# Optimization experiments

Measured on AMD Instinct MI355X. Metric: run time of the kernel, lower is better.

## Reference

```python
import jax, jax.numpy as jnp
import numpy as np

NUM_HEADS = 8
BN_EPS = 1e-3  # keras BatchNormalization default epsilon


def setup_inputs() -> dict:
    key = jax.random.key(0)
    ks = jax.random.split(key, 4)
    B, N, C, s, H = 8, 1024, 3, 16, NUM_HEADS
    dim = s * s * C  # 768
    return {
        "x": jax.random.normal(ks[0], (B, N, dim), jnp.float32),
        "qconv_w": jax.random.normal(ks[1], (3, 3, C, C), jnp.float32) * 0.1,  # HWIO, shared q/k/v (source bug, faithful)
        "reatten_w": jax.random.normal(ks[2], (H, H), jnp.float32) * 0.2,      # 1x1 conv mixing heads
        "reatten_b": jnp.zeros((H,), jnp.float32),
        "bn_gamma": jnp.ones((H,), jnp.float32),
        "bn_beta": jnp.zeros((H,), jnp.float32),
        "bn_mean": jnp.zeros((H,), jnp.float32),
        "bn_var": jnp.ones((H,), jnp.float32),
        "proj_w": jax.random.normal(ks[3], (dim, dim), jnp.float32) * 0.02,
        "proj_b": jnp.zeros((dim,), jnp.float32),
    }


def reference(x, qconv_w, reatten_w, reatten_b, bn_gamma, bn_beta, bn_mean, bn_var, proj_w, proj_b):
    H = NUM_HEADS
    B, N, P = x.shape
    C = qconv_w.shape[2]
    s = int(np.sqrt(P // C))
    hd = P // H
    scale = hd ** -0.5

    # unflatten: tokens become conv batch; 3x3 same conv, no bias
    xim = x.reshape(B * N, s, s, C)
    y = jax.lax.conv_general_dilated(
        xim, qconv_w, window_strides=(1, 1), padding='SAME',
        dimension_numbers=('NHWC', 'HWIO', 'NHWC'))
    # source applies qconv2d for q, k AND v -> identical projections
    q = y.reshape(B, N, H, hd).transpose(0, 2, 1, 3)  # [B,H,N,hd]

    attn = jax.nn.softmax(jnp.einsum('bhnd,bhmd->bhnm', q, q) * scale, axis=-1)

    # re-attention: 1x1 conv across heads + inference batchnorm (per head channel), reatten_scale=1.0
    re = jnp.einsum('bhnm,hg->bgnm', attn, reatten_w) + reatten_b[None, :, None, None]
    st = lambda a: a[None, :, None, None]
    attn_next = (re - st(bn_mean)) * st(bn_gamma) / jnp.sqrt(st(bn_var) + BN_EPS) + st(bn_beta)

    out = jnp.einsum('bgnm,bgmd->bngd', attn_next, q).reshape(B, N, P)
    xo = out @ proj_w + proj_b
    return (xo, attn_next)
```

## Files before the change

kernel.cpp:

```cpp
#include <hip/hip_runtime.h>

#define NB 8
#define NN 1024
#define NH 8
#define HD 96
#define DIM 768

typedef __bf16 bf16x8 __attribute__((ext_vector_type(8)));
typedef float f32x4 __attribute__((ext_vector_type(4)));
typedef unsigned short u16x8 __attribute__((ext_vector_type(8)));

__device__ __forceinline__ ushort f2bf(float f) {
  uint u = __float_as_uint(f);
  u += 0x7fffu + ((u >> 16) & 1u);
  return (ushort)(u >> 16);
}
__device__ __forceinline__ float bf2f(ushort u) {
  return __uint_as_float(((uint)u) << 16);
}

__global__ __launch_bounds__(256) void k_prep_w(const float* __restrict__ pw,
                                                ushort* __restrict__ wT) {
  __shared__ ushort tile[64][72];
  int d0 = blockIdx.x * 64;
  int j0 = blockIdx.y * 64;
  int t = threadIdx.x;
  {
    int r = t >> 2;
    int ch = (t & 3) * 16;
    const float* src = pw + (size_t)(d0 + r) * DIM + j0 + ch;
#pragma unroll
    for (int i = 0; i < 16; i += 4) {
      float4 v = *(const float4*)(src + i);
      tile[ch + i + 0][r] = f2bf(v.x);
      tile[ch + i + 1][r] = f2bf(v.y);
      tile[ch + i + 2][r] = f2bf(v.z);
      tile[ch + i + 3][r] = f2bf(v.w);
    }
  }
  __syncthreads();
  {
    int j = t >> 2;
    int ch = (t & 3) * 16;
    union { ushort u[16]; uint4 v[2]; } tmp;
#pragma unroll
    for (int i = 0; i < 16; ++i) tmp.u[i] = tile[j][ch + i];
    uint4* dst = (uint4*)(wT + (size_t)(j0 + j) * DIM + d0 + ch);
    dst[0] = tmp.v[0]; dst[1] = tmp.v[1];
  }
}

__global__ __launch_bounds__(256) void k_conv(const float* __restrict__ x,
                                              const float* __restrict__ w,
                                              ushort* __restrict__ q) {
  __shared__ float xs[768];
  __shared__ float ws[81];
  __shared__ ushort os[768];
  int token = blockIdx.x;
  int t = threadIdx.x;
  const float4* xin = (const float4*)(x + (size_t)token * DIM);
  if (t < 192) ((float4*)xs)[t] = xin[t];
  if (t < 81) ws[t] = w[t];
  __syncthreads();
  int r = t >> 4, c = t & 15;
  float a0 = 0.f, a1 = 0.f, a2 = 0.f;
#pragma unroll
  for (int dr = 0; dr < 3; ++dr) {
    int rr = r + dr - 1;
    bool rok = (rr >= 0) & (rr < 16);
#pragma unroll
    for (int dc = 0; dc < 3; ++dc) {
      int cc = c + dc - 1;
      bool ok = rok & (cc >= 0) & (cc < 16);
#pragma unroll
      for (int ci = 0; ci < 3; ++ci) {
        int idx = ok ? (rr * 16 + cc) * 3 + ci : 0;
        float xv = xs[idx];
        xv = ok ? xv : 0.f;
        const float* wp = ws + ((dr * 3 + dc) * 3 + ci) * 3;
        a0 += xv * wp[0]; a1 += xv * wp[1]; a2 += xv * wp[2];
      }
    }
  }
  os[t * 3 + 0] = f2bf(a0);
  os[t * 3 + 1] = f2bf(a1);
  os[t * 3 + 2] = f2bf(a2);
  __syncthreads();
  uint4* dst = (uint4*)(q + (size_t)token * DIM);
  if (t < 96) dst[t] = ((const uint4*)os)[t];
}

__global__ __launch_bounds__(256) void k_transpose_q(const ushort* __restrict__ q,
                                                     ushort* __restrict__ qT) {
  __shared__ ushort tile[64][72];
  int bb = blockIdx.z;
  int n0 = blockIdx.x * 64;
  int d0 = blockIdx.y * 64;
  int t = threadIdx.x;
  {
    int r = t >> 2;
    int cq = (t & 3) * 16;
    const ushort* src = q + ((size_t)(bb * NN) + n0 + r) * DIM + d0 + cq;
    uint4 v0 = *(const uint4*)src;
    uint4 v1 = *(const uint4*)(src + 8);
    *(uint4*)&tile[r][cq] = v0;
    *(uint4*)&tile[r][cq + 8] = v1;
  }
  __syncthreads();
  {
    int d = t >> 2;
    int nch = (t & 3) * 16;
    union { ushort u[16]; uint4 v[2]; } tmp;
#pragma unroll
    for (int j = 0; j < 16; ++j) tmp.u[j] = tile[nch + j][d];
    uint4* dst = (uint4*)(qT + ((size_t)(bb * DIM) + d0 + d) * NN + n0 + nch);
    dst[0] = tmp.v[0]; dst[1] = tmp.v[1];
  }
}

__global__ __launch_bounds__(128) void k_colsum(const ushort* __restrict__ q,
                                                float* __restrict__ cs) {
  int bb = blockIdx.y;
  int c = blockIdx.x * 128 + threadIdx.x;
  const ushort* p = q + (size_t)bb * NN * DIM + c;
  float s = 0.f;
#pragma unroll 16
  for (int n = 0; n < NN; ++n) s += bf2f(p[(size_t)n * DIM]);
  cs[bb * DIM + c] = s;
}

__global__ __launch_bounds__(256) void k_rowsum(const ushort* __restrict__ q,
                                                float* __restrict__ invb) {
  const int lin = blockIdx.x;
  const int bb = lin & 7;
  const int idx = lin >> 3;
  const int hh = idx & 7;
  const int ng = idx >> 3;
  const int t = threadIdx.x;
  const int wv = t >> 6, lane = t & 63;
  const int lm = lane & 15, lg = lane >> 4;
  const int n0 = ng * 128 + wv * 32;
  const float scale = 0.10206207261596575f;

  const ushort* qb = q + (size_t)bb * NN * DIM;
  const ushort* kb = qb + hh * HD + (size_t)lm * DIM + lg * 8;

  bf16x8 qf[2][3];
#pragma unroll
  for (int nf = 0; nf < 2; ++nf)
#pragma unroll
    for (int ks = 0; ks < 3; ++ks)
      qf[nf][ks] = *(const bf16x8*)(qb + (size_t)(n0 + nf * 16 + lm) * DIM
                                     + hh * HD + ks * 32 + lg * 8);

  float rs[2][4] = {};
  for (int mt = 0; mt < 16; ++mt) {
    const int m0 = mt * 64;
#pragma unroll
    for (int mf = 0; mf < 4; ++mf) {
      const ushort* kp = kb + (size_t)(m0 + mf * 16) * DIM;
      bf16x8 k0 = *(const bf16x8*)(kp);
      bf16x8 k1 = *(const bf16x8*)(kp + 32);
      bf16x8 k2 = *(const bf16x8*)(kp + 64);
      f32x4 s0 = {}, s1 = {};
      s0 = __builtin_amdgcn_mfma_f32_16x16x32_bf16(qf[0][0], k0, s0, 0, 0, 0);
      s0 = __builtin_amdgcn_mfma_f32_16x16x32_bf16(qf[0][1], k1, s0, 0, 0, 0);
      s0 = __builtin_amdgcn_mfma_f32_16x16x32_bf16(qf[0][2], k2, s0, 0, 0, 0);
      s1 = __builtin_amdgcn_mfma_f32_16x16x32_bf16(qf[1][0], k0, s1, 0, 0, 0);
      s1 = __builtin_amdgcn_mfma_f32_16x16x32_bf16(qf[1][1], k1, s1, 0, 0, 0);
      s1 = __builtin_amdgcn_mfma_f32_16x16x32_bf16(qf[1][2], k2, s1, 0, 0, 0);
#pragma unroll
      for (int r = 0; r < 4; ++r) {
        rs[0][r] += __expf(s0[r] * scale);
        rs[1][r] += __expf(s1[r] * scale);
      }
    }
  }
#pragma unroll
  for (int nf = 0; nf < 2; ++nf)
#pragma unroll
    for (int r = 0; r < 4; ++r) {
      float s = rs[nf][r];
      s += __shfl_xor(s, 1); s += __shfl_xor(s, 2);
      s += __shfl_xor(s, 4); s += __shfl_xor(s, 8);
      if (lm == 0)
        invb[(size_t)(bb * 8 + hh) * NN + n0 + nf * 16 + lg * 4 + r] = 1.f / s;
    }
}

__global__ __launch_bounds__(512, 2) void k_attn_pv(
    const ushort* __restrict__ q, const ushort* __restrict__ qT,
    const float* __restrict__ invb, const float* __restrict__ rw,
    const float* __restrict__ gamma, const float* __restrict__ beta,
    const float* __restrict__ mean, const float* __restrict__ var,
    const float* __restrict__ rb,
    float* __restrict__ attn, float* __restrict__ pacc) {
  __shared__ ushort P[2][16384];

  const int lin = blockIdx.x;
  const int bb = lin & 7;
  const int idx = lin >> 3;
  const int nt = idx >> 1;
  const int mh = idx & 1;
  const int n0 = nt * 32;
  const int mbase = mh * 512;
  const int t = threadIdx.x;
  const int w = t >> 6, lane = t & 63;
  const int lm = lane & 15, lg = lane >> 4;
  const float scale = 0.10206207261596575f;

  float wreg[8];
#pragma unroll
  for (int h = 0; h < 8; ++h) wreg[h] = rw[h * 8 + w];
  const float effs = gamma[w] * __frsqrt_rn(var[w] + 1e-3f);
  const float effb = (rb[w] - mean[w]) * effs + beta[w];

  const ushort* qb = q + (size_t)bb * NN * DIM;
  const ushort* vb = qT + (size_t)bb * DIM * NN;
  const ushort* kb = qb + w * HD + (size_t)lm * DIM + lg * 8;

  bf16x8 qf[2][3];
#pragma unroll
  for (int nf = 0; nf < 2; ++nf)
#pragma unroll
    for (int ks = 0; ks < 3; ++ks)
      qf[nf][ks] = *(const bf16x8*)(qb + (size_t)(n0 + nf * 16 + lm) * DIM
                                     + w * HD + ks * 32 + lg * 8);
  float inv[2][4];
#pragma unroll
  for (int nf = 0; nf < 2; ++nf)
#pragma unroll
    for (int r = 0; r < 4; ++r)
      inv[nf][r] = invb[(size_t)(bb * 8 + w) * NN + n0 + nf * 16 + lg * 4 + r];

  f32x4 oacc[2][6] = {};

  for (int mt = 0; mt < 8; ++mt) {
    const int m0 = mbase + mt * 64;
    char* Pc = (char*)P + (mt & 1) * 32768;
#pragma unroll
    for (int mf = 0; mf < 4; ++mf) {
      const ushort* kp = kb + (size_t)(m0 + mf * 16) * DIM;
      bf16x8 k0 = *(const bf16x8*)(kp);
      bf16x8 k1 = *(const bf16x8*)(kp + 32);
      bf16x8 k2 = *(const bf16x8*)(kp + 64);
      f32x4 s0 = {}, s1 = {};
      s0 = __builtin_amdgcn_mfma_f32_16x16x32_bf16(qf[0][0], k0, s0, 0, 0, 0);
      s0 = __builtin_amdgcn_mfma_f32_16x16x32_bf16(qf[0][1], k1, s0, 0, 0, 0);
      s0 = __builtin_amdgcn_mfma_f32_16x16x32_bf16(qf[0][2], k2, s0, 0, 0, 0);
      s1 = __builtin_amdgcn_mfma_f32_16x16x32_bf16(qf[1][0], k0, s1, 0, 0, 0);
      s1 = __builtin_amdgcn_mfma_f32_16x16x32_bf16(qf[1][1], k1, s1, 0, 0, 0);
      s1 = __builtin_amdgcn_mfma_f32_16x16x32_bf16(qf[1][2], k2, s1, 0, 0, 0);
      const int mb = 2 * (mf * 16 + lm);
#pragma unroll
      for (int r = 0; r < 4; ++r) {
        int n = lg * 4 + r;
        int sw = (n & 7) << 4;
        float e0 = __expf(s0[r] * scale) * inv[0][r];
        *(ushort*)(Pc + w * 4096 + n * 128 + (mb ^ sw)) = f2bf(e0);
        float e1 = __expf(s1[r] * scale) * inv[1][r];
        *(ushort*)(Pc + w * 4096 + (n + 16) * 128 + (mb ^ sw)) = f2bf(e1);
      }
    }
    __syncthreads();
    bf16x8 pmf[2][2];
#pragma unroll
    for (int nf = 0; nf < 2; ++nf) {
      int n = nf * 16 + lm;
      int swz = (n & 7) << 4;
#pragma unroll
      for (int ks = 0; ks < 2; ++ks) {
        int rbase = n * 128 + ((2 * (ks * 32 + lg * 8)) ^ swz);
        float mix[8];
#pragma unroll
        for (int j = 0; j < 8; ++j) mix[j] = 0.f;
#pragma unroll
        for (int h = 0; h < 8; ++h) {
          u16x8 pu = *(const u16x8*)(Pc + h * 4096 + rbase);
#pragma unroll
          for (int j = 0; j < 8; ++j) mix[j] += bf2f(pu[j]) * wreg[h];
        }
        f32x4 o0, o1;
        o0[0] = mix[0] * effs + effb; o0[1] = mix[1] * effs + effb;
        o0[2] = mix[2] * effs + effb; o0[3] = mix[3] * effs + effb;
        o1[0] = mix[4] * effs + effb; o1[1] = mix[5] * effs + effb;
        o1[2] = mix[6] * effs + effb; o1[3] = mix[7] * effs + effb;
        size_t arow = ((size_t)(bb * 8 + w) * NN + (n0 + n)) * NN + m0 + ks * 32 + lg * 8;
        __builtin_nontemporal_store(o0, (f32x4*)(attn + arow));
        __builtin_nontemporal_store(o1, (f32x4*)(attn + arow + 4));
        u16x8 pk;
#pragma unroll
        for (int j = 0; j < 8; ++j) pk[j] = f2bf(mix[j]);
        pmf[nf][ks] = *(bf16x8*)&pk;
      }
    }
#pragma unroll
    for (int ks = 0; ks < 2; ++ks) {
      bf16x8 vf[6];
#pragma unroll
      for (int df = 0; df < 6; ++df)
        vf[df] = *(const bf16x8*)(vb + (size_t)(w * HD + df * 16 + lm) * NN
                                   + m0 + ks * 32 + lg * 8);
#pragma unroll
      for (int df = 0; df < 6; ++df) {
        oacc[0][df] = __builtin_amdgcn_mfma_f32_16x16x32_bf16(pmf[0][ks], vf[df], oacc[0][df], 0, 0, 0);
        oacc[1][df] = __builtin_amdgcn_mfma_f32_16x16x32_bf16(pmf[1][ks], vf[df], oacc[1][df], 0, 0, 0);
      }
    }
  }

#pragma unroll
  for (int df = 0; df < 6; ++df) {
    int col = w * HD + df * 16 + lm;
#pragma unroll
    for (int nf = 0; nf < 2; ++nf)
#pragma unroll
      for (int r = 0; r < 4; ++r) {
        int row = n0 + nf * 16 + lg * 4 + r;
        unsafeAtomicAdd(&pacc[(size_t)(bb * NN + row) * DIM + col], oacc[nf][df][r]);
      }
  }
}

__global__ __launch_bounds__(256) void k_sumfix(const float* __restrict__ pacc,
    const float* __restrict__ cs,
    const float* __restrict__ gamma, const float* __restrict__ beta,
    const float* __restrict__ mean, const float* __restrict__ var,
    const float* __restrict__ rb, ushort* __restrict__ outb) {
  size_t base = ((size_t)blockIdx.x * 256 + threadIdx.x) * 4;
  int col = (int)(base % DIM);
  int brow = (int)(base / DIM);
  int bb = brow >> 10;
  int g = col / 96;
  float effs = gamma[g] * __frsqrt_rn(var[g] + 1e-3f);
  float effb = (rb[g] - mean[g]) * effs + beta[g];
  f32x4 p = *(const f32x4*)(pacc + base);
  f32x4 c = *(const f32x4*)(cs + bb * DIM + col);
  ushort4 o;
  o.x = f2bf(p[0] * effs + effb * c[0]);
  o.y = f2bf(p[1] * effs + effb * c[1]);
  o.z = f2bf(p[2] * effs + effb * c[2]);
  o.w = f2bf(p[3] * effs + effb * c[3]);
  *(ushort4*)(outb + base) = o;
}

__global__ __launch_bounds__(256) void k_proj(const ushort* __restrict__ outb,
                                              const ushort* __restrict__ wT,
                                              const float* __restrict__ pb,
                                              float* __restrict__ xo) {
  __shared__ ushort As[128][72];
  __shared__ ushort Bs[128][72];
  int m0 = blockIdx.x * 128;
  int j0 = blockIdx.y * 128;
  int t = threadIdx.x;
  int wv = t >> 6, lane = t & 63;
  int wr = (wv >> 1) * 64, wc = (wv & 1) * 64;
  int lm = lane & 15, lg = lane >> 4;
  f32x4 acc[4][4] = {};
  for (int kk = 0; kk < 12; ++kk) {
    int k0 = kk * 64;
    __syncthreads();
    for (int i = t; i < 1024; i += 256) {
      int row = i >> 3;
      int c = (i & 7) * 8;
      *(uint4*)&As[row][c] = *(const uint4*)(outb + (size_t)(m0 + row) * DIM + k0 + c);
      *(uint4*)&Bs[row][c] = *(const uint4*)(wT + (size_t)(j0 + row) * DIM + k0 + c);
    }
    __syncthreads();
#pragma unroll
    for (int ks = 0; ks < 2; ++ks) {
      bf16x8 af[4], bfr[4];
#pragma unroll
      for (int mi = 0; mi < 4; ++mi)
        af[mi] = *(const bf16x8*)&As[wr + mi * 16 + lm][ks * 32 + lg * 8];
#pragma unroll
      for (int ni = 0; ni < 4; ++ni)
        bfr[ni] = *(const bf16x8*)&Bs[wc + ni * 16 + lm][ks * 32 + lg * 8];
#pragma unroll
      for (int mi = 0; mi < 4; ++mi)
#pragma unroll
        for (int ni = 0; ni < 4; ++ni)
          acc[mi][ni] = __builtin_amdgcn_mfma_f32_16x16x32_bf16(af[mi], bfr[ni], acc[mi][ni], 0, 0, 0);
    }
  }
#pragma unroll
  for (int ni = 0; ni < 4; ++ni) {
    int col = j0 + wc + ni * 16 + lm;
    float bias = pb[col];
#pragma unroll
    for (int mi = 0; mi < 4; ++mi)
#pragma unroll
      for (int r = 0; r < 4; ++r) {
        int row = m0 + wr + mi * 16 + lg * 4 + r;
        xo[(size_t)row * DIM + col] = acc[mi][ni][r] + bias;
      }
  }
}

extern "C" void kernel_launch(void* const* d_in, const int* in_sizes, int n_in,
                              void* d_out, int out_size, void* d_ws, size_t ws_size,
                              hipStream_t stream) {
  (void)in_sizes; (void)n_in; (void)out_size; (void)ws_size;
  const float* x       = (const float*)d_in[0];
  const float* qconv_w = (const float*)d_in[1];
  const float* rw      = (const float*)d_in[2];
  const float* rb      = (const float*)d_in[3];
  const float* gamma   = (const float*)d_in[4];
  const float* beta    = (const float*)d_in[5];
  const float* mean    = (const float*)d_in[6];
  const float* var     = (const float*)d_in[7];
  const float* pw      = (const float*)d_in[8];
  const float* pb      = (const float*)d_in[9];

  float* xo   = (float*)d_out;
  float* attn = xo + (size_t)NB * NN * DIM;

  char* ws = (char*)d_ws;
  ushort* q    = (ushort*)(ws);
  ushort* qT   = (ushort*)(ws + 12582912);
  ushort* wT   = (ushort*)(ws + 25165824);
  ushort* outb = (ushort*)(ws + 26345472);
  float*  csum = (float*)(ws + 38928384);
  float*  invb = (float*)(ws + 38952960);
  float*  pacc = (float*)(ws + 39215104);

  hipMemsetAsync(pacc, 0, (size_t)NB * NN * DIM * sizeof(float), stream);
  hipLaunchKernelGGL(k_prep_w, dim3(12, 12), dim3(256), 0, stream, pw, wT);
  hipLaunchKernelGGL(k_conv, dim3(NB * NN), dim3(256), 0, stream, x, qconv_w, q);
  hipLaunchKernelGGL(k_transpose_q, dim3(16, 12, NB), dim3(256), 0, stream, q, qT);
  hipLaunchKernelGGL(k_colsum, dim3(6, NB), dim3(128), 0, stream, q, csum);
  hipLaunchKernelGGL(k_rowsum, dim3(512), dim3(256), 0, stream, q, invb);
  hipLaunchKernelGGL(k_attn_pv, dim3(512), dim3(512), 0, stream, q, qT, invb,
                     rw, gamma, beta, mean, var, rb, attn, pacc);
  hipLaunchKernelGGL(k_sumfix, dim3(6144), dim3(256), 0, stream, pacc, csum,
                     gamma, beta, mean, var, rb, outb);
  hipLaunchKernelGGL(k_proj, dim3(64, 6), dim3(256), 0, stream, outb, wT, pb, xo);
}
```

Before: 309.1 us.

## Split fused attention-PV into separate attn and PV GEMM kernels, drop atomics

Removes the PV product from the attention kernel, along with the atomic accumulation into a float buffer, the memset, the column-sum and the sumfix kernels. A new k_pv kernel re-reads the written fp32 attn_next tensor, converts it to bf16 and runs a tiled GEMM against qT, writing outb directly. The row-sum kernel is retiled to 16 rows per wave with more blocks and batched K loads. This trades atomics and extra passes for re-reading a 256 MB attention matrix from memory, which adds considerable bandwidth cost.

```diff
diff --git a/kernel.cpp b/kernel.cpp
--- a/kernel.cpp
+++ b/kernel.cpp
@@ -118,83 +118,66 @@
   }
 }
 
-__global__ __launch_bounds__(128) void k_colsum(const ushort* __restrict__ q,
-                                                float* __restrict__ cs) {
-  int bb = blockIdx.y;
-  int c = blockIdx.x * 128 + threadIdx.x;
-  const ushort* p = q + (size_t)bb * NN * DIM + c;
-  float s = 0.f;
-#pragma unroll 16
-  for (int n = 0; n < NN; ++n) s += bf2f(p[(size_t)n * DIM]);
-  cs[bb * DIM + c] = s;
-}
-
-__global__ __launch_bounds__(256) void k_rowsum(const ushort* __restrict__ q,
-                                                float* __restrict__ invb) {
+__global__ __launch_bounds__(256, 4) void k_rowsum(const ushort* __restrict__ q,
+                                                   float* __restrict__ invb) {
   const int lin = blockIdx.x;
   const int bb = lin & 7;
-  const int idx = lin >> 3;
-  const int hh = idx & 7;
-  const int ng = idx >> 3;
+  const int hh = (lin >> 3) & 7;
+  const int ng = lin >> 6;
   const int t = threadIdx.x;
   const int wv = t >> 6, lane = t & 63;
   const int lm = lane & 15, lg = lane >> 4;
-  const int n0 = ng * 128 + wv * 32;
+  const int n0 = ng * 64 + wv * 16;
   const float scale = 0.10206207261596575f;
 
   const ushort* qb = q + (size_t)bb * NN * DIM;
   const ushort* kb = qb + hh * HD + (size_t)lm * DIM + lg * 8;
 
-  bf16x8 qf[2][3];
-#pragma unroll
-  for (int nf = 0; nf < 2; ++nf)
-#pragma unroll
-    for (int ks = 0; ks < 3; ++ks)
-      qf[nf][ks] = *(const bf16x8*)(qb + (size_t)(n0 + nf * 16 + lm) * DIM
-                                     + hh * HD + ks * 32 + lg * 8);
-
-  float rs[2][4] = {};
+  bf16x8 qf[3];
+#pragma unroll
+  for (int ks = 0; ks < 3; ++ks)
+    qf[ks] = *(const bf16x8*)(qb + (size_t)(n0 + lm) * DIM + hh * HD + ks * 32 + lg * 8);
+
+  float rs[4] = {};
   for (int mt = 0; mt < 16; ++mt) {
     const int m0 = mt * 64;
+    bf16x8 kf[3][4];
 #pragma unroll
     for (int mf = 0; mf < 4; ++mf) {
       const ushort* kp = kb + (size_t)(m0 + mf * 16) * DIM;
-      bf16x8 k0 = *(const bf16x8*)(kp);
-      bf16x8 k1 = *(const bf16x8*)(kp + 32);
-      bf16x8 k2 = *(const bf16x8*)(kp + 64);
-      f32x4 s0 = {}, s1 = {};
-      s0 = __builtin_amdgcn_mfma_f32_16x16x32_bf16(qf[0][0], k0, s0, 0, 0, 0);
-      s0 = __builtin_amdgcn_mfma_f32_16x16x32_bf16(qf[0][1], k1, s0, 0, 0, 0);
-      s0 = __builtin_amdgcn_mfma_f32_16x16x32_bf16(qf[0][2], k2, s0, 0, 0, 0);
-      s1 = __builtin_amdgcn_mfma_f32_16x16x32_bf16(qf[1][0], k0, s1, 0, 0, 0);
-      s1 = __builtin_amdgcn_mfma_f32_16x16x32_bf16(qf[1][1], k1, s1, 0, 0, 0);
-      s1 = __builtin_amdgcn_mfma_f32_16x16x32_bf16(qf[1][2], k2, s1, 0, 0, 0);
-#pragma unroll
-      for (int r = 0; r < 4; ++r) {
-        rs[0][r] += __expf(s0[r] * scale);
-        rs[1][r] += __expf(s1[r] * scale);
-      }
-    }
-  }
-#pragma unroll
-  for (int nf = 0; nf < 2; ++nf)
-#pragma unroll
-    for (int r = 0; r < 4; ++r) {
-      float s = rs[nf][r];
-      s += __shfl_xor(s, 1); s += __shfl_xor(s, 2);
-      s += __shfl_xor(s, 4); s += __shfl_xor(s, 8);
-      if (lm == 0)
-        invb[(size_t)(bb * 8 + hh) * NN + n0 + nf * 16 + lg * 4 + r] = 1.f / s;
-    }
-}
-
-__global__ __launch_bounds__(512, 2) void k_attn_pv(
-    const ushort* __restrict__ q, const ushort* __restrict__ qT,
-    const float* __restrict__ invb, const float* __restrict__ rw,
+      kf[0][mf] = *(const bf16x8*)(kp);
+      kf[1][mf] = *(const bf16x8*)(kp + 32);
+      kf[2][mf] = *(const bf16x8*)(kp + 64);
+    }
+    f32x4 sacc[4] = {};
+#pragma unroll
+    for (int mf = 0; mf < 4; ++mf) {
+      sacc[mf] = __builtin_amdgcn_mfma_f32_16x16x32_bf16(qf[0], kf[0][mf], sacc[mf], 0, 0, 0);
+      sacc[mf] = __builtin_amdgcn_mfma_f32_16x16x32_bf16(qf[1], kf[1][mf], sacc[mf], 0, 0, 0);
+      sacc[mf] = __builtin_amdgcn_mfma_f32_16x16x32_bf16(qf[2], kf[2][mf], sacc[mf], 0, 0, 0);
+    }
+#pragma unroll
+    for (int mf = 0; mf < 4; ++mf)
+#pragma unroll
+      for (int r = 0; r < 4; ++r)
+        rs[r] += __expf(sacc[mf][r] * scale);
+  }
+#pragma unroll
+  for (int r = 0; r < 4; ++r) {
+    float s = rs[r];
+    s += __shfl_xor(s, 1); s += __shfl_xor(s, 2);
+    s += __shfl_xor(s, 4); s += __shfl_xor(s, 8);
+    if (lm == 0)
+      invb[(size_t)(bb * 8 + hh) * NN + n0 + lg * 4 + r] = 1.f / s;
+  }
+}
+
+__global__ __launch_bounds__(512, 4) void k_attn(
+    const ushort* __restrict__ q, const float* __restrict__ invb,
+    const float* __restrict__ rw, const float* __restrict__ rb,
     const float* __restrict__ gamma, const float* __restrict__ beta,
     const float* __restrict__ mean, const float* __restrict__ var,
-    const float* __restrict__ rb,
-    float* __restrict__ attn, float* __restrict__ pacc) {
+    float* __restrict__ attn) {
   __shared__ ushort P[2][16384];
 
   const int lin = blockIdx.x;
@@ -216,7 +199,6 @@
   const float effb = (rb[w] - mean[w]) * effs + beta[w];
 
   const ushort* qb = q + (size_t)bb * NN * DIM;
-  const ushort* vb = qT + (size_t)bb * DIM * NN;
   const ushort* kb = qb + w * HD + (size_t)lm * DIM + lg * 8;
 
   bf16x8 qf[2][3];
@@ -232,8 +214,6 @@
 #pragma unroll
     for (int r = 0; r < 4; ++r)
       inv[nf][r] = invb[(size_t)(bb * 8 + w) * NN + n0 + nf * 16 + lg * 4 + r];
-
-  f32x4 oacc[2][6] = {};
 
   for (int mt = 0; mt < 8; ++mt) {
     const int m0 = mbase + mt * 64;
@@ -263,7 +243,6 @@
       }
     }
     __syncthreads();
-    bf16x8 pmf[2][2];
 #pragma unroll
     for (int nf = 0; nf < 2; ++nf) {
       int n = nf * 16 + lm;
@@ -288,60 +267,68 @@
         size_t arow = ((size_t)(bb * 8 + w) * NN + (n0 + n)) * NN + m0 + ks * 32 + lg * 8;
         __builtin_nontemporal_store(o0, (f32x4*)(attn + arow));
         __builtin_nontemporal_store(o1, (f32x4*)(attn + arow + 4));
-        u16x8 pk;
-#pragma unroll
-        for (int j = 0; j < 8; ++j) pk[j] = f2bf(mix[j]);
-        pmf[nf][ks] = *(bf16x8*)&pk;
       }
     }
+  }
+}
+
+__global__ __launch_bounds__(256) void k_pv(const float* __restrict__ attn,
+                                            const ushort* __restrict__ qT,
+                                            ushort* __restrict__ outb) {
+  __shared__ ushort As[128][72];
+  __shared__ ushort Bs[96][72];
+  int bg = blockIdx.y;
+  int bb = bg >> 3, g = bg & 7;
+  int n0 = blockIdx.x * 128;
+  int t = threadIdx.x;
+  const float* abase = attn + ((size_t)bg * NN + n0) * NN;
+  const ushort* vbase = qT + ((size_t)bb * DIM + g * HD) * NN;
+  int wv = t >> 6, lane = t & 63;
+  int lm = lane & 15, lg = lane >> 4;
+  f32x4 acc[2][6] = {};
+  for (int kk = 0; kk < 16; ++kk) {
+    int k0 = kk * 64;
+    __syncthreads();
+    for (int i = t; i < 2048; i += 256) {
+      int row = i >> 4;
+      int c = (i & 15) * 4;
+      float4 vv = *(const float4*)(abase + (size_t)row * NN + k0 + c);
+      ushort4 u;
+      u.x = f2bf(vv.x); u.y = f2bf(vv.y); u.z = f2bf(vv.z); u.w = f2bf(vv.w);
+      *(ushort4*)&As[row][c] = u;
+    }
+    for (int i = t; i < 768; i += 256) {
+      int d = i >> 3;
+      int c = (i & 7) * 8;
+      *(uint4*)&Bs[d][c] = *(const uint4*)(vbase + (size_t)d * NN + k0 + c);
+    }
+    __syncthreads();
 #pragma unroll
     for (int ks = 0; ks < 2; ++ks) {
-      bf16x8 vf[6];
-#pragma unroll
-      for (int df = 0; df < 6; ++df)
-        vf[df] = *(const bf16x8*)(vb + (size_t)(w * HD + df * 16 + lm) * NN
-                                   + m0 + ks * 32 + lg * 8);
-#pragma unroll
-      for (int df = 0; df < 6; ++df) {
-        oacc[0][df] = __builtin_amdgcn_mfma_f32_16x16x32_bf16(pmf[0][ks], vf[df], oacc[0][df], 0, 0, 0);
-        oacc[1][df] = __builtin_amdgcn_mfma_f32_16x16x32_bf16(pmf[1][ks], vf[df], oacc[1][df], 0, 0, 0);
+      bf16x8 af[2], bfr[6];
+#pragma unroll
+      for (int mi = 0; mi < 2; ++mi)
+        af[mi] = *(const bf16x8*)&As[wv * 32 + mi * 16 + lm][ks * 32 + lg * 8];
+#pragma unroll
+      for (int ni = 0; ni < 6; ++ni)
+        bfr[ni] = *(const bf16x8*)&Bs[ni * 16 + lm][ks * 32 + lg * 8];
+#pragma unroll
+      for (int mi = 0; mi < 2; ++mi)
+#pragma unroll
+        for (int ni = 0; ni < 6; ++ni)
+          acc[mi][ni] = __builtin_amdgcn_mfma_f32_16x16x32_bf16(af[mi], bfr[ni], acc[mi][ni], 0, 0, 0);
+    }
+  }
+#pragma unroll
+  for (int mi = 0; mi < 2; ++mi)
+#pragma unroll
+    for (int ni = 0; ni < 6; ++ni)
+#pragma unroll
+      for (int r = 0; r < 4; ++r) {
+        int row = n0 + wv * 32 + mi * 16 + lg * 4 + r;
+        int col = g * HD + ni * 16 + lm;
+        outb[(size_t)(bb * NN + row) * DIM + col] = f2bf(acc[mi][ni][r]);
       }
-    }
-  }
-
-#pragma unroll
-  for (int df = 0; df < 6; ++df) {
-    int col = w * HD + df * 16 + lm;
-#pragma unroll
-    for (int nf = 0; nf < 2; ++nf)
-#pragma unroll
-      for (int r = 0; r < 4; ++r) {
-        int row = n0 + nf * 16 + lg * 4 + r;
-        unsafeAtomicAdd(&pacc[(size_t)(bb * NN + row) * DIM + col], oacc[nf][df][r]);
-      }
-  }
-}
-
-__global__ __launch_bounds__(256) void k_sumfix(const float* __restrict__ pacc,
-    const float* __restrict__ cs,
-    const float* __restrict__ gamma, const float* __restrict__ beta,
-    const float* __restrict__ mean, const float* __restrict__ var,
-    const float* __restrict__ rb, ushort* __restrict__ outb) {
-  size_t base = ((size_t)blockIdx.x * 256 + threadIdx.x) * 4;
-  int col = (int)(base % DIM);
-  int brow = (int)(base / DIM);
-  int bb = brow >> 10;
-  int g = col / 96;
-  float effs = gamma[g] * __frsqrt_rn(var[g] + 1e-3f);
-  float effb = (rb[g] - mean[g]) * effs + beta[g];
-  f32x4 p = *(const f32x4*)(pacc + base);
-  f32x4 c = *(const f32x4*)(cs + bb * DIM + col);
-  ushort4 o;
-  o.x = f2bf(p[0] * effs + effb * c[0]);
-  o.y = f2bf(p[1] * effs + effb * c[1]);
-  o.z = f2bf(p[2] * effs + effb * c[2]);
-  o.w = f2bf(p[3] * effs + effb * c[3]);
-  *(ushort4*)(outb + base) = o;
 }
 
 __global__ __launch_bounds__(256) void k_proj(const ushort* __restrict__ outb,
@@ -420,19 +407,14 @@
   ushort* qT   = (ushort*)(ws + 12582912);
   ushort* wT   = (ushort*)(ws + 25165824);
   ushort* outb = (ushort*)(ws + 26345472);
-  float*  csum = (float*)(ws + 38928384);
-  float*  invb = (float*)(ws + 38952960);
-  float*  pacc = (float*)(ws + 39215104);
-
-  hipMemsetAsync(pacc, 0, (size_t)NB * NN * DIM * sizeof(float), stream);
+  float*  invb = (float*)(ws + 38928384);
+
   hipLaunchKernelGGL(k_prep_w, dim3(12, 12), dim3(256), 0, stream, pw, wT);
   hipLaunchKernelGGL(k_conv, dim3(NB * NN), dim3(256), 0, stream, x, qconv_w, q);
   hipLaunchKernelGGL(k_transpose_q, dim3(16, 12, NB), dim3(256), 0, stream, q, qT);
-  hipLaunchKernelGGL(k_colsum, dim3(6, NB), dim3(128), 0, stream, q, csum);
-  hipLaunchKernelGGL(k_rowsum, dim3(512), dim3(256), 0, stream, q, invb);
-  hipLaunchKernelGGL(k_attn_pv, dim3(512), dim3(512), 0, stream, q, qT, invb,
-                     rw, gamma, beta, mean, var, rb, attn, pacc);
-  hipLaunchKernelGGL(k_sumfix, dim3(6144), dim3(256), 0, stream, pacc, csum,
-                     gamma, beta, mean, var, rb, outb);
+  hipLaunchKernelGGL(k_rowsum, dim3(1024), dim3(256), 0, stream, q, invb);
+  hipLaunchKernelGGL(k_attn, dim3(512), dim3(512), 0, stream, q, invb,
+                     rw, rb, gamma, beta, mean, var, attn);
+  hipLaunchKernelGGL(k_pv, dim3(8, NB * NH), dim3(256), 0, stream, attn, qT, outb);
   hipLaunchKernelGGL(k_proj, dim3(64, 6), dim3(256), 0, stream, outb, wT, pb, xo);
 }
```

Measured after the change: 345.2 us. 11.7% more time.
